# Performance work log

Hardware: AMD Instinct MI355X
Metric: run time of the kernel (lower is better)

Reference implementation:

```python
import jax, jax.numpy as jnp
import numpy as np

FG_WEIGHT = 13.0
BG_WEIGHT = 1.0
DOWNSAMPLE_FACTOR = 1

B, H, W = 16, 768, 2048
N_PER_IMG = 32


def setup_inputs() -> dict:
    key = jax.random.key(0)
    k_loss, kx1, ky1, kw, kh = jax.random.split(key, 5)
    loss = jax.random.normal(k_loss, (B, H, W), dtype=jnp.float32)
    n_total = B * N_PER_IMG
    # realistic in-frame boxes: x1 < x2 <= W, y1 < y2 <= H
    x1 = jax.random.uniform(kx1, (n_total,), minval=0.0, maxval=W - 256.0)
    y1 = jax.random.uniform(ky1, (n_total,), minval=0.0, maxval=H - 192.0)
    bw = jax.random.uniform(kw, (n_total,), minval=16.0, maxval=256.0)
    bh = jax.random.uniform(kh, (n_total,), minval=16.0, maxval=192.0)
    gt_boxes2d = jnp.stack([x1, y1, x1 + bw, y1 + bh], axis=1).astype(jnp.float32)
    return {"loss": loss, "gt_boxes2d": gt_boxes2d, "num_gt_per_img": N_PER_IMG}


def _compute_fg_mask(gt_boxes2d, num_gt_per_img, b, h, w):
    # boxes: (B*N, 4) -> (B, N, 4); floor mins, ceil maxes (matches torch .long() raster)
    boxes = gt_boxes2d / DOWNSAMPLE_FACTOR
    boxes = boxes.reshape(b, num_gt_per_img, 4)
    u1 = jnp.floor(boxes[..., 0]).astype(jnp.int32)  # (B, N)
    v1 = jnp.floor(boxes[..., 1]).astype(jnp.int32)
    u2 = jnp.ceil(boxes[..., 2]).astype(jnp.int32)
    v2 = jnp.ceil(boxes[..., 3]).astype(jnp.int32)
    rows = jnp.arange(h)  # (H,)
    cols = jnp.arange(w)  # (W,)
    # separable membership: (B, N, H) and (B, N, W)
    row_in = (rows[None, None, :] >= v1[..., None]) & (rows[None, None, :] < v2[..., None])
    col_in = (cols[None, None, :] >= u1[..., None]) & (cols[None, None, :] < u2[..., None])
    # union over boxes via a small matmul instead of a (B,N,H,W) intermediate
    overlap = jnp.einsum("bnh,bnw->bhw", row_in.astype(jnp.float32), col_in.astype(jnp.float32))
    return overlap > 0.0  # (B, H, W) bool


def reference(loss, gt_boxes2d, num_gt_per_img):
    b, h, w = loss.shape
    fg_mask = _compute_fg_mask(gt_boxes2d, num_gt_per_img, b, h, w)
    weights = jnp.where(fg_mask, FG_WEIGHT, BG_WEIGHT).astype(loss.dtype)
    # fg_mask.sum() + bg_mask.sum() == total pixel count
    num_pixels = jnp.asarray(b * h * w, dtype=loss.dtype)
    # fg_loss + bg_loss == sum(loss * weights) / num_pixels (masks partition the image)
    return jnp.sum(loss * weights) / num_pixels
```

## Files before the change

### kernel.cpp

```cpp
#include <hip/hip_runtime.h>

constexpr int Bv = 16, Hv = 768, Wv = 2048;
constexpr int ROWS_PER_BLOCK = 4;
constexpr int NROWS   = Bv * Hv;
constexpr int NBLOCKS = NROWS / ROWS_PER_BLOCK;
constexpr int MAXN    = 256;

__global__ __launch_bounds__(256) void balancer_main(
    const float* __restrict__ loss,
    const float* __restrict__ boxes,
    const int*   __restrict__ num_gt,
    double*      __restrict__ partials)
{
    const int tid  = threadIdx.x;
    const int row0 = blockIdx.x * ROWS_PER_BLOCK;
    const int b    = row0 / Hv;
    const int h0   = row0 - b * Hv;
    const int n    = num_gt[0];

    float4 vbuf[ROWS_PER_BLOCK][2];
    const float4* base = (const float4*)(loss + (size_t)row0 * Wv);
    #pragma unroll
    for (int r = 0; r < ROWS_PER_BLOCK; ++r) {
        #pragma unroll
        for (int it = 0; it < 2; ++it)
            vbuf[r][it] = base[r * (Wv / 4) + it * 256 + tid];
    }

    __shared__ int  s_cnt[ROWS_PER_BLOCK];
    __shared__ int2 s_uv[ROWS_PER_BLOCK][MAXN];

    if (tid < ROWS_PER_BLOCK) s_cnt[tid] = 0;
    __syncthreads();

    for (int i = tid; i < n && i < MAXN; i += 256) {
        const float4 bx = ((const float4*)boxes)[b * n + i];
        const int u1 = (int)floorf(bx.x);
        const int v1 = (int)floorf(bx.y);
        const int u2 = (int)ceilf(bx.z);
        const int v2 = (int)ceilf(bx.w);
        #pragma unroll
        for (int r = 0; r < ROWS_PER_BLOCK; ++r) {
            const int h = h0 + r;
            if (h >= v1 && h < v2) {
                const int pos = atomicAdd(&s_cnt[r], 1);
                s_uv[r][pos] = make_int2(u1, u2);
            }
        }
    }
    __syncthreads();

    float sum = 0.0f;
    #pragma unroll
    for (int r = 0; r < ROWS_PER_BLOCK; ++r) {
        const int m = s_cnt[r];
        #pragma unroll
        for (int it = 0; it < 2; ++it) {
            const float4 v  = vbuf[r][it];
            const int    c0 = (it * 256 + tid) * 4;
            bool f0 = false, f1 = false, f2 = false, f3 = false;
            for (int i = 0; i < m; ++i) {
                const int2 uv = s_uv[r][i];
                f0 |= (c0     >= uv.x) & (c0     < uv.y);
                f1 |= (c0 + 1 >= uv.x) & (c0 + 1 < uv.y);
                f2 |= (c0 + 2 >= uv.x) & (c0 + 2 < uv.y);
                f3 |= (c0 + 3 >= uv.x) & (c0 + 3 < uv.y);
            }
            sum += v.x * (f0 ? 13.0f : 1.0f);
            sum += v.y * (f1 ? 13.0f : 1.0f);
            sum += v.z * (f2 ? 13.0f : 1.0f);
            sum += v.w * (f3 ? 13.0f : 1.0f);
        }
    }

    for (int off = 32; off > 0; off >>= 1)
        sum += __shfl_down(sum, off, 64);

    __shared__ float s_wsum[4];
    const int lane = tid & 63;
    const int wid  = tid >> 6;
    if (lane == 0) s_wsum[wid] = sum;
    __syncthreads();
    if (tid == 0) {
        double d = 0.0;
        #pragma unroll
        for (int wq = 0; wq < 4; ++wq) d += (double)s_wsum[wq];
        partials[blockIdx.x] = d;
    }
}

__global__ __launch_bounds__(256) void balancer_reduce(
    const double* __restrict__ partials, float* __restrict__ out)
{
    const int tid = threadIdx.x;
    double s = 0.0;
    for (int i = tid; i < NBLOCKS; i += 256) s += partials[i];
    for (int off = 32; off > 0; off >>= 1)
        s += __shfl_down(s, off, 64);
    __shared__ double sh[4];
    if ((tid & 63) == 0) sh[tid >> 6] = s;
    __syncthreads();
    if (tid == 0) {
        const double t = sh[0] + sh[1] + sh[2] + sh[3];
        out[0] = (float)(t / (double)((long long)Bv * Hv * Wv));
    }
}

extern "C" void kernel_launch(void* const* d_in, const int* in_sizes, int n_in,
                              void* d_out, int out_size, void* d_ws, size_t ws_size,
                              hipStream_t stream) {
    const float* loss   = (const float*)d_in[0];
    const float* boxes  = (const float*)d_in[1];
    const int*   num_gt = (const int*)d_in[2];
    double*      partials = (double*)d_ws;
    float*       out      = (float*)d_out;

    balancer_main<<<NBLOCKS, 256, 0, stream>>>(loss, boxes, num_gt, partials);
    balancer_reduce<<<1, 256, 0, stream>>>(partials, out);
}
```

Before: 159.9 us.

## Fuse final reduction via last-block ticket and use wave ballot for box culling

Replaces the shared-memory box list, its atomics and two block barriers with a per-wave ballot over up to 64 boxes, broadcasting box extents with shuffles. The separate reduce kernel is folded into the main kernel: a global ticket counter elects the last block to sum all partials, which removes one launch. Loss loads become nontemporal. The ticket adds a global atomic per block and relies on a modulo wraparound across calls, and a slow fallback path remains for more than 64 boxes per image.

```diff
diff --git a/kernel.cpp b/kernel.cpp
--- a/kernel.cpp
+++ b/kernel.cpp
@@ -4,72 +4,113 @@
 constexpr int ROWS_PER_BLOCK = 4;
 constexpr int NROWS   = Bv * Hv;
 constexpr int NBLOCKS = NROWS / ROWS_PER_BLOCK;
-constexpr int MAXN    = 256;
 
-__global__ __launch_bounds__(256) void balancer_main(
+typedef float f32x4 __attribute__((ext_vector_type(4)));
+
+__device__ unsigned long long g_ticket = 0ull;
+
+__global__ __launch_bounds__(256) void balancer_fused(
     const float* __restrict__ loss,
     const float* __restrict__ boxes,
     const int*   __restrict__ num_gt,
-    double*      __restrict__ partials)
+    double*      __restrict__ partials,
+    float*       __restrict__ out)
 {
     const int tid  = threadIdx.x;
+    const int lane = tid & 63;
+    const int wid  = tid >> 6;
     const int row0 = blockIdx.x * ROWS_PER_BLOCK;
     const int b    = row0 / Hv;
     const int h0   = row0 - b * Hv;
     const int n    = num_gt[0];
 
-    float4 vbuf[ROWS_PER_BLOCK][2];
-    const float4* base = (const float4*)(loss + (size_t)row0 * Wv);
+    f32x4 vbuf[ROWS_PER_BLOCK][2];
+    const f32x4* base4 = (const f32x4*)(loss + (size_t)row0 * Wv);
     #pragma unroll
     for (int r = 0; r < ROWS_PER_BLOCK; ++r) {
         #pragma unroll
         for (int it = 0; it < 2; ++it)
-            vbuf[r][it] = base[r * (Wv / 4) + it * 256 + tid];
+            vbuf[r][it] = __builtin_nontemporal_load(&base4[r * (Wv / 4) + it * 256 + tid]);
     }
 
-    __shared__ int  s_cnt[ROWS_PER_BLOCK];
-    __shared__ int2 s_uv[ROWS_PER_BLOCK][MAXN];
+    float sum = 0.0f;
+    const int c0 = tid * 4;
+    const int c1 = 1024 + tid * 4;
 
-    if (tid < ROWS_PER_BLOCK) s_cnt[tid] = 0;
-    __syncthreads();
+    if (n <= 64) {
+        int u1 = 0, u2 = 0, v1 = 0, v2 = 0;
+        if (lane < n) {
+            const f32x4 bx = ((const f32x4*)boxes)[b * n + lane];
+            u1 = (int)floorf(bx.x);
+            v1 = (int)floorf(bx.y);
+            u2 = (int)ceilf(bx.z);
+            v2 = (int)ceilf(bx.w);
+        }
 
-    for (int i = tid; i < n && i < MAXN; i += 256) {
-        const float4 bx = ((const float4*)boxes)[b * n + i];
-        const int u1 = (int)floorf(bx.x);
-        const int v1 = (int)floorf(bx.y);
-        const int u2 = (int)ceilf(bx.z);
-        const int v2 = (int)ceilf(bx.w);
         #pragma unroll
         for (int r = 0; r < ROWS_PER_BLOCK; ++r) {
             const int h = h0 + r;
-            if (h >= v1 && h < v2) {
-                const int pos = atomicAdd(&s_cnt[r], 1);
-                s_uv[r][pos] = make_int2(u1, u2);
+            unsigned long long mask = __ballot(h >= v1 && h < v2);
+            bool fa0 = false, fa1 = false, fa2 = false, fa3 = false;
+            bool fb0 = false, fb1 = false, fb2 = false, fb3 = false;
+            while (mask) {
+                const int src = __builtin_ctzll(mask);
+                mask &= mask - 1;
+                const int a = __shfl(u1, src, 64);
+                const int e = __shfl(u2, src, 64);
+                fa0 |= (c0     >= a) & (c0     < e);
+                fa1 |= (c0 + 1 >= a) & (c0 + 1 < e);
+                fa2 |= (c0 + 2 >= a) & (c0 + 2 < e);
+                fa3 |= (c0 + 3 >= a) & (c0 + 3 < e);
+                fb0 |= (c1     >= a) & (c1     < e);
+                fb1 |= (c1 + 1 >= a) & (c1 + 1 < e);
+                fb2 |= (c1 + 2 >= a) & (c1 + 2 < e);
+                fb3 |= (c1 + 3 >= a) & (c1 + 3 < e);
             }
+            const f32x4 va = vbuf[r][0];
+            sum += va.x * (fa0 ? 13.0f : 1.0f);
+            sum += va.y * (fa1 ? 13.0f : 1.0f);
+            sum += va.z * (fa2 ? 13.0f : 1.0f);
+            sum += va.w * (fa3 ? 13.0f : 1.0f);
+            const f32x4 vb = vbuf[r][1];
+            sum += vb.x * (fb0 ? 13.0f : 1.0f);
+            sum += vb.y * (fb1 ? 13.0f : 1.0f);
+            sum += vb.z * (fb2 ? 13.0f : 1.0f);
+            sum += vb.w * (fb3 ? 13.0f : 1.0f);
         }
-    }
-    __syncthreads();
-
-    float sum = 0.0f;
-    #pragma unroll
-    for (int r = 0; r < ROWS_PER_BLOCK; ++r) {
-        const int m = s_cnt[r];
+    } else {
         #pragma unroll
-        for (int it = 0; it < 2; ++it) {
-            const float4 v  = vbuf[r][it];
-            const int    c0 = (it * 256 + tid) * 4;
-            bool f0 = false, f1 = false, f2 = false, f3 = false;
-            for (int i = 0; i < m; ++i) {
-                const int2 uv = s_uv[r][i];
-                f0 |= (c0     >= uv.x) & (c0     < uv.y);
-                f1 |= (c0 + 1 >= uv.x) & (c0 + 1 < uv.y);
-                f2 |= (c0 + 2 >= uv.x) & (c0 + 2 < uv.y);
-                f3 |= (c0 + 3 >= uv.x) & (c0 + 3 < uv.y);
+        for (int r = 0; r < ROWS_PER_BLOCK; ++r) {
+            const int h = h0 + r;
+            bool fa0 = false, fa1 = false, fa2 = false, fa3 = false;
+            bool fb0 = false, fb1 = false, fb2 = false, fb3 = false;
+            for (int i = 0; i < n; ++i) {
+                const f32x4 bx = ((const f32x4*)boxes)[b * n + i];
+                const int v1 = (int)floorf(bx.y);
+                const int v2 = (int)ceilf(bx.w);
+                if (h >= v1 && h < v2) {
+                    const int a = (int)floorf(bx.x);
+                    const int e = (int)ceilf(bx.z);
+                    fa0 |= (c0     >= a) & (c0     < e);
+                    fa1 |= (c0 + 1 >= a) & (c0 + 1 < e);
+                    fa2 |= (c0 + 2 >= a) & (c0 + 2 < e);
+                    fa3 |= (c0 + 3 >= a) & (c0 + 3 < e);
+                    fb0 |= (c1     >= a) & (c1     < e);
+                    fb1 |= (c1 + 1 >= a) & (c1 + 1 < e);
+                    fb2 |= (c1 + 2 >= a) & (c1 + 2 < e);
+                    fb3 |= (c1 + 3 >= a) & (c1 + 3 < e);
+                }
             }
-            sum += v.x * (f0 ? 13.0f : 1.0f);
-            sum += v.y * (f1 ? 13.0f : 1.0f);
-            sum += v.z * (f2 ? 13.0f : 1.0f);
-            sum += v.w * (f3 ? 13.0f : 1.0f);
+            const f32x4 va = vbuf[r][0];
+            sum += va.x * (fa0 ? 13.0f : 1.0f);
+            sum += va.y * (fa1 ? 13.0f : 1.0f);
+            sum += va.z * (fa2 ? 13.0f : 1.0f);
+            sum += va.w * (fa3 ? 13.0f : 1.0f);
+            const f32x4 vb = vbuf[r][1];
+            sum += vb.x * (fb0 ? 13.0f : 1.0f);
+            sum += vb.y * (fb1 ? 13.0f : 1.0f);
+            sum += vb.z * (fb2 ? 13.0f : 1.0f);
+            sum += vb.w * (fb3 ? 13.0f : 1.0f);
         }
     }
 
@@ -77,32 +118,38 @@
         sum += __shfl_down(sum, off, 64);
 
     __shared__ float s_wsum[4];
-    const int lane = tid & 63;
-    const int wid  = tid >> 6;
+    __shared__ bool  s_last;
     if (lane == 0) s_wsum[wid] = sum;
     __syncthreads();
+
     if (tid == 0) {
         double d = 0.0;
         #pragma unroll
         for (int wq = 0; wq < 4; ++wq) d += (double)s_wsum[wq];
-        partials[blockIdx.x] = d;
+        __hip_atomic_store(&partials[blockIdx.x], d,
+                           __ATOMIC_RELAXED, __HIP_MEMORY_SCOPE_AGENT);
+        const unsigned long long t =
+            __hip_atomic_fetch_add(&g_ticket, 1ull,
+                                   __ATOMIC_ACQ_REL, __HIP_MEMORY_SCOPE_AGENT);
+        s_last = ((t % (unsigned long long)NBLOCKS) ==
+                  (unsigned long long)(NBLOCKS - 1));
     }
-}
+    __syncthreads();
 
-__global__ __launch_bounds__(256) void balancer_reduce(
-    const double* __restrict__ partials, float* __restrict__ out)
-{
-    const int tid = threadIdx.x;
-    double s = 0.0;
-    for (int i = tid; i < NBLOCKS; i += 256) s += partials[i];
-    for (int off = 32; off > 0; off >>= 1)
-        s += __shfl_down(s, off, 64);
-    __shared__ double sh[4];
-    if ((tid & 63) == 0) sh[tid >> 6] = s;
-    __syncthreads();
-    if (tid == 0) {
-        const double t = sh[0] + sh[1] + sh[2] + sh[3];
-        out[0] = (float)(t / (double)((long long)Bv * Hv * Wv));
+    if (s_last) {
+        double s = 0.0;
+        for (int i = tid; i < NBLOCKS; i += 256)
+            s += __hip_atomic_load(&partials[i],
+                                   __ATOMIC_RELAXED, __HIP_MEMORY_SCOPE_AGENT);
+        for (int off = 32; off > 0; off >>= 1)
+            s += __shfl_down(s, off, 64);
+        __shared__ double sh[4];
+        if (lane == 0) sh[wid] = s;
+        __syncthreads();
+        if (tid == 0) {
+            const double t = sh[0] + sh[1] + sh[2] + sh[3];
+            out[0] = (float)(t / (double)((long long)Bv * Hv * Wv));
+        }
     }
 }
 
@@ -115,6 +162,5 @@
     double*      partials = (double*)d_ws;
     float*       out      = (float*)d_out;
 
-    balancer_main<<<NBLOCKS, 256, 0, stream>>>(loss, boxes, num_gt, partials);
-    balancer_reduce<<<1, 256, 0, stream>>>(partials, out);
+    balancer_fused<<<NBLOCKS, 256, 0, stream>>>(loss, boxes, num_gt, partials, out);
 }
```

Result: slower. 265.9 us (+66.3%).
